# Kernel optimization log

Hardware: AMD Instinct MI355X
Metric: run time of the kernel (lower is better)

Reference implementation:

```python
import jax, jax.numpy as jnp
import numpy as np

D_MODEL = 2048
N_HEADS = 16
HEAD_DIM = D_MODEL // N_HEADS
ROPE_THETA = 10000.0
B, S = 2, 2048
MAX_POS = 8192


def _rope(x, position_ids):
    # x: [b, h, s, hd]; position_ids: [b, s] int
    half = HEAD_DIM // 2
    inv_freq = 1.0 / (ROPE_THETA ** (jnp.arange(0, HEAD_DIM, 2, dtype=jnp.float32) / HEAD_DIM))  # [half]
    ang = position_ids[..., None].astype(jnp.float32) * inv_freq  # [b, s, half]
    cos = jnp.concatenate([jnp.cos(ang), jnp.cos(ang)], axis=-1)[:, None]  # [b, 1, s, hd]
    sin = jnp.concatenate([jnp.sin(ang), jnp.sin(ang)], axis=-1)[:, None]
    x1, x2 = x[..., :half], x[..., half:]
    rot = jnp.concatenate([-x2, x1], axis=-1)  # rotate_half
    return x * cos + rot * sin


def setup_inputs() -> dict:
    key = jax.random.key(0)
    ks = jax.random.split(key, 6)
    wscale = 1.0 / np.sqrt(D_MODEL)
    x_sparse = jax.random.normal(ks[0], (B, S, D_MODEL), dtype=jnp.float32)
    Wq = jax.random.normal(ks[1], (D_MODEL, D_MODEL), dtype=jnp.float32) * wscale
    Wk = jax.random.normal(ks[2], (D_MODEL, D_MODEL), dtype=jnp.float32) * wscale
    Wv = jax.random.normal(ks[3], (D_MODEL, D_MODEL), dtype=jnp.float32) * wscale
    Wo = jax.random.normal(ks[4], (D_MODEL, D_MODEL), dtype=jnp.float32) * wscale
    position_ids = jnp.sort(jax.random.randint(ks[5], (B, S), 0, MAX_POS), axis=-1).astype(jnp.int64)
    return {"x_sparse": x_sparse, "Wq": Wq, "Wk": Wk, "Wv": Wv, "Wo": Wo, "position_ids": position_ids}


def reference(x_sparse, Wq, Wk, Wv, Wo, position_ids):
    b, s, d = x_sparse.shape

    def heads(W):
        return (x_sparse @ W).reshape(b, s, N_HEADS, HEAD_DIM).transpose(0, 2, 1, 3)  # [b,h,s,hd]

    q = _rope(heads(Wq), position_ids)
    k = _rope(heads(Wk), position_ids)
    v = heads(Wv)

    scores = jnp.einsum('bhqd,bhkd->bhqk', q, k) / np.float32(np.sqrt(HEAD_DIM))
    # dynamic position-based causal mask: pos_i >= pos_j, broadcast over heads
    mask = position_ids[:, None, :, None] >= position_ids[:, None, None, :]  # [b,1,s,s]
    scores = jnp.where(mask, scores, jnp.float32(-1e30))
    attn = jax.nn.softmax(scores, axis=-1)
    out = jnp.einsum('bhqk,bhkd->bhqd', attn, v)  # [b,h,s,hd]
    out = out.transpose(0, 2, 1, 3).reshape(b, s, d)
    return out @ Wo
```

## Files before the change

kernel.cpp:

```cpp
#include <hip/hip_runtime.h>
#include <stdint.h>


typedef unsigned short u16;
typedef unsigned int u32;
typedef __attribute__((ext_vector_type(8))) short bf16x8;
typedef __attribute__((ext_vector_type(4))) float f32x4;

#define SEQ 2048
#define DM 2048
#define NH 16
#define HD 128
#define SM_SCALE 0.08838834764831845f
#define K2LOG 0.12751743f

__device__ __forceinline__ u16 f2bf(float f) {
  union { float f; uint32_t u; } v; v.f = f;
  uint32_t u = v.u + 0x7fffu + ((v.u >> 16) & 1u);
  return (u16)(u >> 16);
}
__device__ __forceinline__ float bf2f(u16 h) {
  union { uint32_t u; float f; } v; v.u = ((uint32_t)h) << 16; return v.f;
}
__device__ __forceinline__ u32 pack2(float a, float b) {
  return (u32)f2bf(a) | ((u32)f2bf(b) << 16);
}
__device__ __forceinline__ u32 pack2_trunc(float a, float b) {
  union { float f; u32 u; } x, y; x.f = a; y.f = b;
  return (x.u >> 16) | (y.u & 0xFFFF0000u);
}

__device__ __forceinline__ void gl2lds16(const void* g, void* l) {
  __builtin_amdgcn_global_load_lds(
      (const __attribute__((address_space(1))) uint32_t*)g,
      (__attribute__((address_space(3))) uint32_t*)l, 16, 0, 0);
}

__global__ __launch_bounds__(256) void cvt_x(const float* __restrict__ x, u16* __restrict__ xb) {
  int i = blockIdx.x * 256 + threadIdx.x;
  float4 v = ((const float4*)x)[i];
  uint2 r;
  r.x = pack2(v.x, v.y);
  r.y = pack2(v.z, v.w);
  ((uint2*)xb)[i] = r;
}

__global__ __launch_bounds__(256) void wtrans(const float* __restrict__ w0, const float* __restrict__ w1,
                                              const float* __restrict__ w2, const float* __restrict__ w3,
                                              u16* __restrict__ dst) {
  const float* W = blockIdx.z == 0 ? w0 : blockIdx.z == 1 ? w1 : blockIdx.z == 2 ? w2 : w3;
  u16* D = dst + (size_t)blockIdx.z * DM * DM;
  int k0 = blockIdx.x * 32, n0 = blockIdx.y * 32;
  __shared__ u16 t[32][33];
  int tx = threadIdx.x, ty = threadIdx.y;
#pragma unroll
  for (int i = 0; i < 32; i += 8)
    t[ty + i][tx] = f2bf(W[(size_t)(k0 + ty + i) * DM + n0 + tx]);
  __syncthreads();
#pragma unroll
  for (int i = 0; i < 32; i += 8)
    D[(size_t)(n0 + ty + i) * DM + k0 + tx] = t[tx][ty + i];
}

__device__ __forceinline__ void gemm_core(const u16* __restrict__ A, const u16* __restrict__ Bt,
                                          int m0, int n0, u16* As, u16* Bs, f32x4 acc[4][4]) {
  int tid = threadIdx.x, lane = tid & 63;
  int l15 = lane & 15, quad = lane >> 4;
  int wave = tid >> 6;
  int wm = (wave >> 1) * 64, wn = (wave & 1) * 64;
  for (int k0 = 0; k0 < DM; k0 += 64) {
#pragma unroll
    for (int i = 0; i < 4; ++i) {
      int s = i * 256 + tid;
      int row = s >> 3, c = (s & 7) ^ (row & 7);
      gl2lds16(&A[(size_t)(m0 + row) * DM + k0 + c * 8], &As[(s & ~63) * 8]);
      gl2lds16(&Bt[(size_t)(n0 + row) * DM + k0 + c * 8], &Bs[(s & ~63) * 8]);
    }
    __syncthreads();
#pragma unroll
    for (int kk = 0; kk < 2; ++kk) {
      bf16x8 af[4], bfr[4];
#pragma unroll
      for (int mt = 0; mt < 4; ++mt) {
        int row = wm + mt * 16 + l15;
        int c = (kk * 4 + quad) ^ (row & 7);
        af[mt] = *(const bf16x8*)&As[row * 64 + c * 8];
      }
#pragma unroll
      for (int nt = 0; nt < 4; ++nt) {
        int row = wn + nt * 16 + l15;
        int c = (kk * 4 + quad) ^ (row & 7);
        bfr[nt] = *(const bf16x8*)&Bs[row * 64 + c * 8];
      }
#pragma unroll
      for (int mt = 0; mt < 4; ++mt)
#pragma unroll
        for (int nt = 0; nt < 4; ++nt)
          acc[mt][nt] = __builtin_amdgcn_mfma_f32_16x16x32_bf16(af[mt], bfr[nt], acc[mt][nt], 0, 0, 0);
    }
    __syncthreads();
  }
}

__global__ __launch_bounds__(256) void qkv_gemm(const u16* __restrict__ X, const u16* __restrict__ Wt,
                                                u16* __restrict__ Qo, u16* __restrict__ Ko,
                                                u16* __restrict__ Vto) {
  __shared__ u16 As[128 * 64];
  __shared__ u16 Bs[128 * 64];
  const u16* Bt = Wt + (size_t)blockIdx.z * DM * DM;
  int n0 = blockIdx.x * 128, m0 = blockIdx.y * 128;
  f32x4 acc[4][4] = {};
  gemm_core(X, Bt, m0, n0, As, Bs, acc);
  int lane = threadIdx.x & 63, wave = threadIdx.x >> 6;
  int l15 = lane & 15, quad = lane >> 4;
  int wm = (wave >> 1) * 64, wn = (wave & 1) * 64;
  if (blockIdx.z == 2) {
    int h = n0 >> 7;
#pragma unroll
    for (int mt = 0; mt < 4; ++mt)
#pragma unroll
      for (int nt = 0; nt < 4; ++nt) {
        int tok = m0 + wm + mt * 16 + quad * 4;
        int d = wn + nt * 16 + l15;
        int b = tok >> 11, sx = tok & (SEQ - 1);
        u16* dp = &Vto[((size_t)(b * NH + h) * HD + d) * SEQ + sx];
        *(u32*)&dp[0] = pack2(acc[mt][nt][0], acc[mt][nt][1]);
        *(u32*)&dp[2] = pack2(acc[mt][nt][2], acc[mt][nt][3]);
      }
  } else {
    u16* C = blockIdx.z == 0 ? Qo : Ko;
#pragma unroll
    for (int mt = 0; mt < 4; ++mt)
#pragma unroll
      for (int nt = 0; nt < 4; ++nt)
#pragma unroll
        for (int r = 0; r < 4; ++r)
          C[(size_t)(m0 + wm + mt * 16 + quad * 4 + r) * DM + n0 + wn + nt * 16 + l15]
              = f2bf(acc[mt][nt][r]);
  }
}

__global__ __launch_bounds__(256) void proj_gemm(const u16* __restrict__ A, const u16* __restrict__ Wt,
                                                 float* __restrict__ C) {
  __shared__ u16 As[128 * 64];
  __shared__ u16 Bs[128 * 64];
  int n0 = blockIdx.x * 128, m0 = blockIdx.y * 128;
  f32x4 acc[4][4] = {};
  gemm_core(A, Wt, m0, n0, As, Bs, acc);
  int lane = threadIdx.x & 63, wave = threadIdx.x >> 6;
  int l15 = lane & 15, quad = lane >> 4;
  int wm = (wave >> 1) * 64, wn = (wave & 1) * 64;
#pragma unroll
  for (int mt = 0; mt < 4; ++mt)
#pragma unroll
    for (int nt = 0; nt < 4; ++nt)
#pragma unroll
      for (int r = 0; r < 4; ++r)
        C[(size_t)(m0 + wm + mt * 16 + quad * 4 + r) * DM + n0 + wn + nt * 16 + l15] = acc[mt][nt][r];
}

__global__ __launch_bounds__(256) void rope_k(u16* __restrict__ Q, u16* __restrict__ K,
                                              const int* __restrict__ pos) {
  uint32_t idx = blockIdx.x * 256 + threadIdx.x;
  int i = idx & 63;
  int h = (idx >> 6) & 15;
  int s = (idx >> 10) & 2047;
  int b = idx >> 21;
  u16* P = (blockIdx.y == 0) ? Q : K;
  int p = pos[b * SEQ + s];
  float inv = exp2f((float)i * -0.20762051f);
  float ang = (float)p * inv;
  float sn, cs;
  sincosf(ang, &sn, &cs);
  size_t base = ((size_t)(b * SEQ + s)) * DM + h * HD;
  float x1 = bf2f(P[base + i]), x2 = bf2f(P[base + 64 + i]);
  P[base + i] = f2bf(x1 * cs - x2 * sn);
  P[base + 64 + i] = f2bf(x2 * cs + x1 * sn);
}

__global__ __launch_bounds__(256) void attn_k(const u16* __restrict__ Q, const u16* __restrict__ K,
                                              const u16* __restrict__ Vt, const int* __restrict__ pos,
                                              u16* __restrict__ AO) {
  __shared__ u16 Ks0[64 * 128], Ks1[64 * 128];
  __shared__ u16 Vs0[128 * 64], Vs1[128 * 64];
  int bx = blockIdx.x, bh = blockIdx.y;
  int b = bh >> 4, h = bh & 15;
  int qt = b ? (15 - bx) : bx;
  int tid = threadIdx.x, lane = tid & 63, wave = tid >> 6;
  int l15 = lane & 15, quad = lane >> 4;
  const int* posb = pos + b * SEQ;
  int qbase = qt * 128 + wave * 16;
  const u16* Kbase = &K[(size_t)(b * SEQ) * DM + h * HD];
  const u16* Vbase = &Vt[(size_t)(b * NH + h) * HD * SEQ];

  auto prefetch = [&](int t, u16* KsD, u16* VsD) {
#pragma unroll
    for (int i = 0; i < 4; ++i) {
      int s = i * 256 + tid;
      int rk = s >> 4, ck = (s & 15) ^ (rk & 15);
      gl2lds16(&Kbase[(size_t)(t * 64 + rk) * DM + ck * 8], &KsD[(s & ~63) * 8]);
      int rv = s >> 3, cv = (s & 7) ^ (rv & 7);
      gl2lds16(&Vbase[(size_t)rv * SEQ + t * 64 + cv * 8], &VsD[(s & ~63) * 8]);
    }
  };
  prefetch(0, Ks0, Vs0);

  bf16x8 qf[2][4];
#pragma unroll
  for (int qi = 0; qi < 2; ++qi)
#pragma unroll
    for (int kk = 0; kk < 4; ++kk)
      qf[qi][kk] = *(const bf16x8*)&Q[(size_t)(b * SEQ + qbase + qi * 64 + l15) * DM
                                      + h * HD + kk * 32 + quad * 8];

  auto ub = [&](int v) {
    int c = 0;
#pragma unroll
    for (int st = 1024; st; st >>= 1)
      if (posb[c + st - 1] <= v) c += st;
    if (c == 2047 && posb[2047] <= v) c = 2048;
    return c;
  };
  int cnt[2];
  cnt[0] = ub(posb[qbase + l15]);
  cnt[1] = ub(posb[qbase + 64 + l15]);
  int cnt_min = ub(posb[qt * 128]);
  int cnt_max = ub(posb[qt * 128 + 127]);
  int ntile = (cnt_max + 63) >> 6;

  float m_i[2] = {-1.0e30f, -1.0e30f}, l_i[2] = {0.0f, 0.0f};
  f32x4 oacc[2][8] = {};

  int base0 = l15 + ((quad & 1) << 5);
  bool hi_sel = (quad >> 1) != 0;

  auto compute = [&](int j0, const u16* KsS, const u16* VsS) {
    f32x4 sacc[2][4] = {};
#pragma unroll
    for (int kk = 0; kk < 4; ++kk) {
      bf16x8 kf[4];
#pragma unroll
      for (int kt = 0; kt < 4; ++kt) {
        int row = kt * 16 + l15;
        int c = (kk * 4 + quad) ^ (row & 15);
        kf[kt] = *(const bf16x8*)&KsS[row * 128 + c * 8];
      }
#pragma unroll
      for (int qi = 0; qi < 2; ++qi)
#pragma unroll
        for (int kt = 0; kt < 4; ++kt)
          sacc[qi][kt] = __builtin_amdgcn_mfma_f32_16x16x32_bf16(kf[kt], qf[qi][kk], sacc[qi][kt], 0, 0, 0);
    }

    bool need_mask = (j0 + 64 > cnt_min);
    u32 pb[2][4][2];
#pragma unroll
    for (int qi = 0; qi < 2; ++qi) {
      if (need_mask) {
        int rel = cnt[qi] - j0;
#pragma unroll
        for (int kt = 0; kt < 4; ++kt)
#pragma unroll
          for (int r = 0; r < 4; ++r)
            if (kt * 16 + quad * 4 + r >= rel) sacc[qi][kt][r] = -1.0e30f;
      }
      float mx = fmaxf(fmaxf(sacc[qi][0][0], sacc[qi][0][1]), fmaxf(sacc[qi][0][2], sacc[qi][0][3]));
#pragma unroll
      for (int kt = 1; kt < 4; ++kt) {
        mx = fmaxf(mx, fmaxf(fmaxf(sacc[qi][kt][0], sacc[qi][kt][1]),
                             fmaxf(sacc[qi][kt][2], sacc[qi][kt][3])));
      }
      mx = fmaxf(mx, __shfl_xor(mx, 16));
      mx = fmaxf(mx, __shfl_xor(mx, 32));
      float mold = m_i[qi];
      float mn = fmaxf(mold, mx);
      if (__any(mn > mold)) {
        float al = exp2f((mold - mn) * K2LOG);
        l_i[qi] *= al;
#pragma unroll
        for (int dt = 0; dt < 8; ++dt) oacc[qi][dt] *= al;
        m_i[qi] = mn;
      }
      float nc = -m_i[qi] * K2LOG;
      float rs = 0.0f;
#pragma unroll
      for (int kt = 0; kt < 4; ++kt) {
        float p0 = exp2f(fmaf(sacc[qi][kt][0], K2LOG, nc));
        float p1 = exp2f(fmaf(sacc[qi][kt][1], K2LOG, nc));
        float p2 = exp2f(fmaf(sacc[qi][kt][2], K2LOG, nc));
        float p3 = exp2f(fmaf(sacc[qi][kt][3], K2LOG, nc));
        rs += (p0 + p1) + (p2 + p3);
        pb[qi][kt][0] = pack2_trunc(p0, p1);
        pb[qi][kt][1] = pack2_trunc(p2, p3);
      }
      rs += __shfl_xor(rs, 16);
      rs += __shfl_xor(rs, 32);
      l_i[qi] += rs;
    }

#pragma unroll
    for (int kk = 0; kk < 2; ++kk) {
      bf16x8 vf[8];
#pragma unroll
      for (int dt = 0; dt < 8; ++dt) {
        int row = dt * 16 + l15;
        int c = (kk * 4 + quad) ^ (row & 7);
        vf[dt] = *(const bf16x8*)&VsS[row * 64 + c * 8];
      }
#pragma unroll
      for (int qi = 0; qi < 2; ++qi) {
        u32 w[4];
#pragma unroll
        for (int wd = 0; wd < 4; ++wd) {
          int src = base0 + ((wd >> 1) << 4);
          u32 va = __shfl(pb[qi][kk * 2 + 0][wd & 1], src);
          u32 vb = __shfl(pb[qi][kk * 2 + 1][wd & 1], src);
          w[wd] = hi_sel ? vb : va;
        }
        union { bf16x8 v; u32 u[4]; } pt;
        pt.u[0] = w[0]; pt.u[1] = w[1]; pt.u[2] = w[2]; pt.u[3] = w[3];
#pragma unroll
        for (int dt = 0; dt < 8; ++dt)
          oacc[qi][dt] = __builtin_amdgcn_mfma_f32_16x16x32_bf16(vf[dt], pt.v, oacc[qi][dt], 0, 0, 0);
      }
    }
  };

  for (int j = 0; j < ntile; j += 2) {
    __syncthreads();
    if (j + 1 < ntile) prefetch(j + 1, Ks1, Vs1);
    compute(j * 64, Ks0, Vs0);
    if (j + 1 >= ntile) break;
    __syncthreads();
    if (j + 2 < ntile) prefetch(j + 2, Ks0, Vs0);
    compute((j + 1) * 64, Ks1, Vs1);
  }

#pragma unroll
  for (int qi = 0; qi < 2; ++qi) {
    float inv = 1.0f / l_i[qi];
    u16* aop = &AO[(size_t)(b * SEQ + qbase + qi * 64 + l15) * DM + h * HD];
#pragma unroll
    for (int dt = 0; dt < 8; ++dt) {
      int col = dt * 16 + quad * 4;
      *(u32*)&aop[col]     = pack2(oacc[qi][dt][0] * inv, oacc[qi][dt][1] * inv);
      *(u32*)&aop[col + 2] = pack2(oacc[qi][dt][2] * inv, oacc[qi][dt][3] * inv);
    }
  }
}

extern "C" void kernel_launch(void* const* d_in, const int* in_sizes, int n_in,
                              void* d_out, int out_size, void* d_ws, size_t ws_size,
                              hipStream_t stream) {
  const float* x  = (const float*)d_in[0];
  const float* Wq = (const float*)d_in[1];
  const float* Wk = (const float*)d_in[2];
  const float* Wv = (const float*)d_in[3];
  const float* Wo = (const float*)d_in[4];
  const int*  pos = (const int*)d_in[5];
  float* out = (float*)d_out;

  u16* ws  = (u16*)d_ws;
  u16* xb  = ws;
  u16* wt  = xb  + (size_t)4096 * 2048;
  u16* qb  = wt  + (size_t)4 * 2048 * 2048;
  u16* kb  = qb  + (size_t)4096 * 2048;
  u16* vtb = kb  + (size_t)4096 * 2048;
  u16* aob = vtb + (size_t)4096 * 2048;

  cvt_x<<<8192, 256, 0, stream>>>(x, xb);
  wtrans<<<dim3(64, 64, 4), dim3(32, 8), 0, stream>>>(Wq, Wk, Wv, Wo, wt);
  qkv_gemm<<<dim3(16, 32, 3), 256, 0, stream>>>(xb, wt, qb, kb, vtb);
  rope_k<<<dim3(16384, 2), 256, 0, stream>>>(qb, kb, pos);
  attn_k<<<dim3(16, 32), 256, 0, stream>>>(qb, kb, vtb, pos, aob);
  proj_gemm<<<dim3(16, 32), 256, 0, stream>>>(aob, wt + (size_t)3 * 2048 * 2048, out);
}
```

Before: 459.3 us.

## Make attention waves independent with direct global loads; use fast RoPE trig

Attention now gives each wave its own 32-row query stripe and (batch,head) pair, with stripes interleaved to balance causal work. K and V fragments are read straight from global memory into registers, so the LDS double buffering and block barriers are gone. The launch grows to 512 blocks with a launch bound of 2 blocks per SM. RoPE computes the angle as a revolution fraction with an error-compensated product and uses __sinf/__cosf instead of sincosf, trading some accuracy for cheaper trig. The risk is that dropping the shared K/V tiles makes each wave reload them from global/L2, increasing memory traffic.

```diff
diff --git a/kernel.cpp b/kernel.cpp
--- a/kernel.cpp
+++ b/kernel.cpp
@@ -168,49 +168,40 @@
   int b = idx >> 21;
   u16* P = (blockIdx.y == 0) ? Q : K;
   int p = pos[b * SEQ + s];
-  float inv = exp2f((float)i * -0.20762051f);
-  float ang = (float)p * inv;
-  float sn, cs;
-  sincosf(ang, &sn, &cs);
+  float inv_rev = exp2f(fmaf((float)i, -0.20762051f, -2.6514961f));
+  float pf = (float)p;
+  float hi = pf * inv_rev;
+  float err = fmaf(pf, inv_rev, -hi);
+  float r = (hi - truncf(hi)) + err;
+  float ang = r * 6.2831853f;
+  float sn = __sinf(ang), cs = __cosf(ang);
   size_t base = ((size_t)(b * SEQ + s)) * DM + h * HD;
   float x1 = bf2f(P[base + i]), x2 = bf2f(P[base + 64 + i]);
   P[base + i] = f2bf(x1 * cs - x2 * sn);
   P[base + 64 + i] = f2bf(x2 * cs + x1 * sn);
 }
 
-__global__ __launch_bounds__(256) void attn_k(const u16* __restrict__ Q, const u16* __restrict__ K,
-                                              const u16* __restrict__ Vt, const int* __restrict__ pos,
-                                              u16* __restrict__ AO) {
-  __shared__ u16 Ks0[64 * 128], Ks1[64 * 128];
-  __shared__ u16 Vs0[128 * 64], Vs1[128 * 64];
-  int bx = blockIdx.x, bh = blockIdx.y;
+__global__ __launch_bounds__(256, 2) void attn_k(const u16* __restrict__ Q, const u16* __restrict__ K,
+                                                 const u16* __restrict__ Vt, const int* __restrict__ pos,
+                                                 u16* __restrict__ AO) {
+  int tid = threadIdx.x, lane = tid & 63, wave = tid >> 6;
+  int J = blockIdx.x * 4 + wave;
+  int bh = J & 31;
+  int t = J >> 5;
+  int stripe = (t < 32) ? (2 * t) : (127 - 2 * t);
   int b = bh >> 4, h = bh & 15;
-  int qt = b ? (15 - bx) : bx;
-  int tid = threadIdx.x, lane = tid & 63, wave = tid >> 6;
   int l15 = lane & 15, quad = lane >> 4;
   const int* posb = pos + b * SEQ;
-  int qbase = qt * 128 + wave * 16;
+  int qbase = stripe * 32;
   const u16* Kbase = &K[(size_t)(b * SEQ) * DM + h * HD];
   const u16* Vbase = &Vt[(size_t)(b * NH + h) * HD * SEQ];
 
-  auto prefetch = [&](int t, u16* KsD, u16* VsD) {
-#pragma unroll
-    for (int i = 0; i < 4; ++i) {
-      int s = i * 256 + tid;
-      int rk = s >> 4, ck = (s & 15) ^ (rk & 15);
-      gl2lds16(&Kbase[(size_t)(t * 64 + rk) * DM + ck * 8], &KsD[(s & ~63) * 8]);
-      int rv = s >> 3, cv = (s & 7) ^ (rv & 7);
-      gl2lds16(&Vbase[(size_t)rv * SEQ + t * 64 + cv * 8], &VsD[(s & ~63) * 8]);
-    }
-  };
-  prefetch(0, Ks0, Vs0);
-
   bf16x8 qf[2][4];
 #pragma unroll
   for (int qi = 0; qi < 2; ++qi)
 #pragma unroll
     for (int kk = 0; kk < 4; ++kk)
-      qf[qi][kk] = *(const bf16x8*)&Q[(size_t)(b * SEQ + qbase + qi * 64 + l15) * DM
+      qf[qi][kk] = *(const bf16x8*)&Q[(size_t)(b * SEQ + qbase + qi * 16 + l15) * DM
                                       + h * HD + kk * 32 + quad * 8];
 
   auto ub = [&](int v) {
@@ -223,9 +214,9 @@
   };
   int cnt[2];
   cnt[0] = ub(posb[qbase + l15]);
-  cnt[1] = ub(posb[qbase + 64 + l15]);
-  int cnt_min = ub(posb[qt * 128]);
-  int cnt_max = ub(posb[qt * 128 + 127]);
+  cnt[1] = ub(posb[qbase + 16 + l15]);
+  int cnt_min = ub(posb[qbase]);
+  int cnt_max = ub(posb[qbase + 31]);
   int ntile = (cnt_max + 63) >> 6;
 
   float m_i[2] = {-1.0e30f, -1.0e30f}, l_i[2] = {0.0f, 0.0f};
@@ -234,23 +225,30 @@
   int base0 = l15 + ((quad & 1) << 5);
   bool hi_sel = (quad >> 1) != 0;
 
-  auto compute = [&](int j0, const u16* KsS, const u16* VsS) {
+  for (int j = 0; j < ntile; ++j) {
+    int j0 = j * 64;
+    bf16x8 kf[4][4];
+#pragma unroll
+    for (int kk = 0; kk < 4; ++kk)
+#pragma unroll
+      for (int kt = 0; kt < 4; ++kt)
+        kf[kk][kt] = *(const bf16x8*)&Kbase[(size_t)(j0 + kt * 16 + l15) * DM + kk * 32 + quad * 8];
+
     f32x4 sacc[2][4] = {};
 #pragma unroll
-    for (int kk = 0; kk < 4; ++kk) {
-      bf16x8 kf[4];
-#pragma unroll
-      for (int kt = 0; kt < 4; ++kt) {
-        int row = kt * 16 + l15;
-        int c = (kk * 4 + quad) ^ (row & 15);
-        kf[kt] = *(const bf16x8*)&KsS[row * 128 + c * 8];
-      }
+    for (int kk = 0; kk < 4; ++kk)
 #pragma unroll
       for (int qi = 0; qi < 2; ++qi)
 #pragma unroll
         for (int kt = 0; kt < 4; ++kt)
-          sacc[qi][kt] = __builtin_amdgcn_mfma_f32_16x16x32_bf16(kf[kt], qf[qi][kk], sacc[qi][kt], 0, 0, 0);
-    }
+          sacc[qi][kt] = __builtin_amdgcn_mfma_f32_16x16x32_bf16(kf[kk][kt], qf[qi][kk], sacc[qi][kt], 0, 0, 0);
+
+    bf16x8 vf[2][8];
+#pragma unroll
+    for (int kk2 = 0; kk2 < 2; ++kk2)
+#pragma unroll
+      for (int dt = 0; dt < 8; ++dt)
+        vf[kk2][dt] = *(const bf16x8*)&Vbase[(size_t)(dt * 16 + l15) * SEQ + j0 + kk2 * 32 + quad * 8];
 
     bool need_mask = (j0 + 64 > cnt_min);
     u32 pb[2][4][2];
@@ -266,10 +264,9 @@
       }
       float mx = fmaxf(fmaxf(sacc[qi][0][0], sacc[qi][0][1]), fmaxf(sacc[qi][0][2], sacc[qi][0][3]));
 #pragma unroll
-      for (int kt = 1; kt < 4; ++kt) {
+      for (int kt = 1; kt < 4; ++kt)
         mx = fmaxf(mx, fmaxf(fmaxf(sacc[qi][kt][0], sacc[qi][kt][1]),
                              fmaxf(sacc[qi][kt][2], sacc[qi][kt][3])));
-      }
       mx = fmaxf(mx, __shfl_xor(mx, 16));
       mx = fmaxf(mx, __shfl_xor(mx, 32));
       float mold = m_i[qi];
@@ -299,47 +296,30 @@
     }
 
 #pragma unroll
-    for (int kk = 0; kk < 2; ++kk) {
-      bf16x8 vf[8];
-#pragma unroll
-      for (int dt = 0; dt < 8; ++dt) {
-        int row = dt * 16 + l15;
-        int c = (kk * 4 + quad) ^ (row & 7);
-        vf[dt] = *(const bf16x8*)&VsS[row * 64 + c * 8];
-      }
+    for (int kk2 = 0; kk2 < 2; ++kk2) {
 #pragma unroll
       for (int qi = 0; qi < 2; ++qi) {
         u32 w[4];
 #pragma unroll
         for (int wd = 0; wd < 4; ++wd) {
           int src = base0 + ((wd >> 1) << 4);
-          u32 va = __shfl(pb[qi][kk * 2 + 0][wd & 1], src);
-          u32 vb = __shfl(pb[qi][kk * 2 + 1][wd & 1], src);
+          u32 va = __shfl(pb[qi][kk2 * 2 + 0][wd & 1], src);
+          u32 vb = __shfl(pb[qi][kk2 * 2 + 1][wd & 1], src);
           w[wd] = hi_sel ? vb : va;
         }
         union { bf16x8 v; u32 u[4]; } pt;
         pt.u[0] = w[0]; pt.u[1] = w[1]; pt.u[2] = w[2]; pt.u[3] = w[3];
 #pragma unroll
         for (int dt = 0; dt < 8; ++dt)
-          oacc[qi][dt] = __builtin_amdgcn_mfma_f32_16x16x32_bf16(vf[dt], pt.v, oacc[qi][dt], 0, 0, 0);
-      }
-    }
-  };
-
-  for (int j = 0; j < ntile; j += 2) {
-    __syncthreads();
-    if (j + 1 < ntile) prefetch(j + 1, Ks1, Vs1);
-    compute(j * 64, Ks0, Vs0);
-    if (j + 1 >= ntile) break;
-    __syncthreads();
-    if (j + 2 < ntile) prefetch(j + 2, Ks0, Vs0);
-    compute((j + 1) * 64, Ks1, Vs1);
+          oacc[qi][dt] = __builtin_amdgcn_mfma_f32_16x16x32_bf16(vf[kk2][dt], pt.v, oacc[qi][dt], 0, 0, 0);
+      }
+    }
   }
 
 #pragma unroll
   for (int qi = 0; qi < 2; ++qi) {
     float inv = 1.0f / l_i[qi];
-    u16* aop = &AO[(size_t)(b * SEQ + qbase + qi * 64 + l15) * DM + h * HD];
+    u16* aop = &AO[(size_t)(b * SEQ + qbase + qi * 16 + l15) * DM + h * HD];
 #pragma unroll
     for (int dt = 0; dt < 8; ++dt) {
       int col = dt * 16 + quad * 4;
@@ -372,6 +352,6 @@
   wtrans<<<dim3(64, 64, 4), dim3(32, 8), 0, stream>>>(Wq, Wk, Wv, Wo, wt);
   qkv_gemm<<<dim3(16, 32, 3), 256, 0, stream>>>(xb, wt, qb, kb, vtb);
   rope_k<<<dim3(16384, 2), 256, 0, stream>>>(qb, kb, pos);
-  attn_k<<<dim3(16, 32), 256, 0, stream>>>(qb, kb, vtb, pos, aob);
+  attn_k<<<dim3(512), 256, 0, stream>>>(qb, kb, vtb, pos, aob);
   proj_gemm<<<dim3(16, 32), 256, 0, stream>>>(aob, wt + (size_t)3 * 2048 * 2048, out);
 }
```

New measurement: 453.0 us. About the same (-1.4%).
